# Kernel optimization log

Measured on AMD Instinct MI355X. Metric: run time of the kernel, lower is better.

Reference implementation:

```python
import jax, jax.numpy as jnp
import numpy as np

N = 50000
ALPHA = 0.1
LAMDA = 0.5


def setup_inputs() -> dict:
    key = jax.random.key(0)
    ks = jax.random.split(key, 8)
    E, IN, H, C, L = 800000, 512, 128, 40, 8
    features = jax.random.normal(ks[0], (N, IN), dtype=jnp.float32)
    edge_index = jax.random.randint(ks[1], (2, E), 0, N, dtype=jnp.int32)
    norm_A = jax.random.uniform(ks[2], (E,), dtype=jnp.float32) * 0.1
    w_fc0 = jax.random.normal(ks[3], (IN, H), dtype=jnp.float32) / np.sqrt(IN)
    b_fc0 = jnp.zeros((H,), dtype=jnp.float32)
    conv_w = jax.random.normal(ks[4], (L, H, H), dtype=jnp.float32) / np.sqrt(H)
    w_fc1 = jax.random.normal(ks[5], (H, C), dtype=jnp.float32) / np.sqrt(H)
    b_fc1 = jnp.zeros((C,), dtype=jnp.float32)
    return {"features": features, "edge_index": edge_index, "norm_A": norm_A,
            "w_fc0": w_fc0, "b_fc0": b_fc0, "conv_w": conv_w,
            "w_fc1": w_fc1, "b_fc1": b_fc1}


def _spmm(edge_index, w, x):
    # y[dst] += w_e * x[src]  over all edges; x: [N, H]
    src, dst = edge_index[0], edge_index[1]
    msgs = x[src] * w[:, None]                      # [E, H]
    return jax.ops.segment_sum(msgs, dst, num_segments=N)


def reference(features, edge_index, norm_A, w_fc0, b_fc0, conv_w, w_fc1, b_fc1):
    # dropout p=0.0 -> identity
    x = jax.nn.relu(features @ w_fc0 + b_fc0)       # [N, H]
    h0 = x
    L = conv_w.shape[0]
    for i in range(L):
        l = i + 1
        beta = jnp.log(LAMDA / l + 1.0).astype(x.dtype)
        hi = _spmm(edge_index, norm_A, x)           # Â x
        support = (1.0 - ALPHA) * hi + ALPHA * h0   # initial residual
        # identity mapping: beta * (support W) + (1-beta) * support
        x = jax.nn.relu(beta * (support @ conv_w[i]) + (1.0 - beta) * support)
    return x @ w_fc1 + b_fc1                        # [N, C]
```

## Files before the change

### kernel.cpp

```cpp
#include <hip/hip_runtime.h>
#include <hip/hip_bf16.h>
#include <math.h>

#define N_NODES 50000
#define M_PAD   50048
#define E_EDGES 800000
#define IN_DIM  512
#define HDIM    128
#define CDIM    40
#define LAYERS  8
#define NB      196

typedef __attribute__((ext_vector_type(8))) short short8;
typedef __attribute__((ext_vector_type(4))) short short4v;
typedef __attribute__((ext_vector_type(4))) float floatx4;
typedef unsigned short ushort_t;

__device__ inline float bf2f(unsigned short u) {
    return __uint_as_float(((unsigned)u) << 16);
}
__device__ inline unsigned short f2bf(float v) {
    __hip_bfloat16 b = __float2bfloat16(v);
    return *reinterpret_cast<unsigned short*>(&b);
}


__global__ void hist_kernel(const int* __restrict__ dst, int* __restrict__ cnt) {
    int i = blockIdx.x * blockDim.x + threadIdx.x;
    if (i < E_EDGES) atomicAdd(&cnt[dst[i]], 1);
}

__global__ void scanA(const int* __restrict__ cnt, int* __restrict__ bsum) {
    __shared__ int sm[256];
    int t = threadIdx.x, i = blockIdx.x * 256 + t;
    sm[t] = (i < N_NODES) ? cnt[i] : 0;
    __syncthreads();
    for (int d = 128; d > 0; d >>= 1) {
        if (t < d) sm[t] += sm[t + d];
        __syncthreads();
    }
    if (t == 0) bsum[blockIdx.x] = sm[0];
}

__global__ void scanB(const int* __restrict__ bsum, int* __restrict__ boff) {
    __shared__ int sm[256];
    int t = threadIdx.x;
    sm[t] = (t < NB) ? bsum[t] : 0;
    __syncthreads();
    for (int d = 1; d < 256; d <<= 1) {
        int v = (t >= d) ? sm[t - d] : 0;
        __syncthreads();
        sm[t] += v;
        __syncthreads();
    }
    if (t < NB) boff[t] = (t > 0) ? sm[t - 1] : 0;
}

__global__ void scanC(const int* __restrict__ cnt, const int* __restrict__ boff,
                      int* __restrict__ row_start, int* __restrict__ cursor) {
    __shared__ int sm[256];
    int t = threadIdx.x, i = blockIdx.x * 256 + t;
    int v = (i < N_NODES) ? cnt[i] : 0;
    sm[t] = v;
    __syncthreads();
    for (int d = 1; d < 256; d <<= 1) {
        int x = (t >= d) ? sm[t - d] : 0;
        __syncthreads();
        sm[t] += x;
        __syncthreads();
    }
    if (i < N_NODES) {
        int incl = boff[blockIdx.x] + sm[t];
        int excl = incl - v;
        row_start[i] = excl;
        cursor[i]    = excl;
        if (i == N_NODES - 1) row_start[N_NODES] = incl;
    }
}

__global__ void scatter_kernel(const int* __restrict__ ei, const float* __restrict__ normA,
                               int* __restrict__ cursor, int2* __restrict__ perm) {
    int i = blockIdx.x * blockDim.x + threadIdx.x;
    if (i >= E_EDGES) return;
    int d = ei[E_EDGES + i];
    int idx = atomicAdd(&cursor[d], 1);
    perm[idx] = make_int2(ei[i], __float_as_int(normA[i]));
}


__global__ void prep_weights(const float* __restrict__ W0, const float* __restrict__ convW,
                             const float* __restrict__ W1,
                             ushort_t* __restrict__ Wt0, ushort_t* __restrict__ WtL,
                             ushort_t* __restrict__ Wt1) {
    int i = blockIdx.x * blockDim.x + threadIdx.x;
    if (i < 128 * 512) {
        int n = i >> 9, k = i & 511;
        Wt0[i] = f2bf(W0[k * HDIM + n]);
        return;
    }
    int j = i - 128 * 512;
    if (j < 8 * 128 * 128) {
        int l = j >> 14, rem = j & 16383, n = rem >> 7, k = rem & 127;
        WtL[j] = f2bf(convW[l * 16384 + k * HDIM + n]);
        return;
    }
    int m = j - 8 * 128 * 128;
    if (m < 48 * 128) {
        int n = m >> 7, k = m & 127;
        Wt1[m] = (n < CDIM) ? f2bf(W1[k * CDIM + n]) : (ushort_t)0;
    }
}


__global__ __launch_bounds__(256)
void fc0_mfma(const float* __restrict__ F, const ushort_t* __restrict__ Wt0,
              const float* __restrict__ b0,
              ushort_t* __restrict__ h0b, ushort_t* __restrict__ xab) {
    int t = threadIdx.x;
    int wave = t >> 6, lane = t & 63;
    int quad = lane >> 4, l16 = lane & 15;
    int R0 = blockIdx.x * 128 + wave * 32;

    int r0 = R0 + l16;      if (r0 > N_NODES - 1) r0 = N_NODES - 1;
    int r1 = R0 + 16 + l16; if (r1 > N_NODES - 1) r1 = N_NODES - 1;
    const float* ap0 = F + (size_t)r0 * IN_DIM + quad * 8;
    const float* ap1 = F + (size_t)r1 * IN_DIM + quad * 8;
    const ushort_t* bbase = Wt0 + (size_t)l16 * IN_DIM + quad * 8;

    floatx4 acc0[8], acc1[8];
#pragma unroll
    for (int nt = 0; nt < 8; nt++) {
        acc0[nt] = (floatx4){0.f, 0.f, 0.f, 0.f};
        acc1[nt] = (floatx4){0.f, 0.f, 0.f, 0.f};
    }

    float4 pa00 = *(const float4*)(ap0);
    float4 pa01 = *(const float4*)(ap0 + 4);
    float4 pa10 = *(const float4*)(ap1);
    float4 pa11 = *(const float4*)(ap1 + 4);
    float4 pb00 = *(const float4*)(ap0 + 32);
    float4 pb01 = *(const float4*)(ap0 + 36);
    float4 pb10 = *(const float4*)(ap1 + 32);
    float4 pb11 = *(const float4*)(ap1 + 36);

#pragma unroll
    for (int kk = 0; kk < 16; kk += 2) {
        short8 a0, a1;
        a0[0] = (short)f2bf(pa00.x); a0[1] = (short)f2bf(pa00.y);
        a0[2] = (short)f2bf(pa00.z); a0[3] = (short)f2bf(pa00.w);
        a0[4] = (short)f2bf(pa01.x); a0[5] = (short)f2bf(pa01.y);
        a0[6] = (short)f2bf(pa01.z); a0[7] = (short)f2bf(pa01.w);
        a1[0] = (short)f2bf(pa10.x); a1[1] = (short)f2bf(pa10.y);
        a1[2] = (short)f2bf(pa10.z); a1[3] = (short)f2bf(pa10.w);
        a1[4] = (short)f2bf(pa11.x); a1[5] = (short)f2bf(pa11.y);
        a1[6] = (short)f2bf(pa11.z); a1[7] = (short)f2bf(pa11.w);
        if (kk + 2 < 16) {
            pa00 = *(const float4*)(ap0 + (kk + 2) * 32);
            pa01 = *(const float4*)(ap0 + (kk + 2) * 32 + 4);
            pa10 = *(const float4*)(ap1 + (kk + 2) * 32);
            pa11 = *(const float4*)(ap1 + (kk + 2) * 32 + 4);
        }
#pragma unroll
        for (int nt = 0; nt < 8; nt++) {
            short8 b = *(const short8*)(bbase + (size_t)nt * 16 * IN_DIM + kk * 32);
            acc0[nt] = __builtin_amdgcn_mfma_f32_16x16x32_bf16(a0, b, acc0[nt], 0, 0, 0);
            acc1[nt] = __builtin_amdgcn_mfma_f32_16x16x32_bf16(a1, b, acc1[nt], 0, 0, 0);
        }
        short8 c0, c1;
        c0[0] = (short)f2bf(pb00.x); c0[1] = (short)f2bf(pb00.y);
        c0[2] = (short)f2bf(pb00.z); c0[3] = (short)f2bf(pb00.w);
        c0[4] = (short)f2bf(pb01.x); c0[5] = (short)f2bf(pb01.y);
        c0[6] = (short)f2bf(pb01.z); c0[7] = (short)f2bf(pb01.w);
        c1[0] = (short)f2bf(pb10.x); c1[1] = (short)f2bf(pb10.y);
        c1[2] = (short)f2bf(pb10.z); c1[3] = (short)f2bf(pb10.w);
        c1[4] = (short)f2bf(pb11.x); c1[5] = (short)f2bf(pb11.y);
        c1[6] = (short)f2bf(pb11.z); c1[7] = (short)f2bf(pb11.w);
        if (kk + 3 < 16) {
            pb00 = *(const float4*)(ap0 + (kk + 3) * 32);
            pb01 = *(const float4*)(ap0 + (kk + 3) * 32 + 4);
            pb10 = *(const float4*)(ap1 + (kk + 3) * 32);
            pb11 = *(const float4*)(ap1 + (kk + 3) * 32 + 4);
        }
#pragma unroll
        for (int nt = 0; nt < 8; nt++) {
            short8 b = *(const short8*)(bbase + (size_t)nt * 16 * IN_DIM + (kk + 1) * 32);
            acc0[nt] = __builtin_amdgcn_mfma_f32_16x16x32_bf16(c0, b, acc0[nt], 0, 0, 0);
            acc1[nt] = __builtin_amdgcn_mfma_f32_16x16x32_bf16(c1, b, acc1[nt], 0, 0, 0);
        }
    }

#pragma unroll
    for (int nt = 0; nt < 8; nt++) {
        int col = nt * 16 + l16;
        float bias = b0[col];
#pragma unroll
        for (int r = 0; r < 4; r++) {
            int row = R0 + quad * 4 + r;
            float v = acc0[nt][r] + bias;
            v = v > 0.f ? v : 0.f;
            ushort_t u = f2bf(v);
            h0b[(size_t)row * HDIM + col] = u;
            xab[(size_t)row * HDIM + col] = u;
        }
#pragma unroll
        for (int r = 0; r < 4; r++) {
            int row = R0 + 16 + quad * 4 + r;
            float v = acc1[nt][r] + bias;
            v = v > 0.f ? v : 0.f;
            ushort_t u = f2bf(v);
            h0b[(size_t)row * HDIM + col] = u;
            xab[(size_t)row * HDIM + col] = u;
        }
    }
}


#define SROW 136

__global__ void layer_fused(const int* __restrict__ row_start, const int2* __restrict__ perm,
                            const ushort_t* __restrict__ xb, const ushort_t* __restrict__ h0b,
                            const ushort_t* __restrict__ Wt, ushort_t* __restrict__ X,
                            float beta) {
    __shared__ short sS[64][SROW];
    int t = threadIdx.x;
    int wave = t >> 6, lane = t & 63;
    int slot = lane >> 4, sl = lane & 15;
    int quad = slot, l16 = sl;
    int row0 = blockIdx.x * 64;
    int R0 = row0 + wave * 16;

    int rb = 0;
    if (lane <= 16) {
        int idx = R0 + lane;
        if (idx > N_NODES) idx = N_NODES;
        rb = row_start[idx];
    }

    for (int r = 0; r < 16; r++) {
        int e0 = __shfl(rb, r), e1 = __shfl(rb, r + 1);
        int grow = R0 + r;
        float acc[8];
#pragma unroll
        for (int c = 0; c < 8; c++) acc[c] = 0.f;

        int ebase = e0 + slot;
        int2 m[4];
        short8 v[4];
#pragma unroll
        for (int d = 0; d < 4; d++) {
            int e = ebase + 4 * d;
            m[d] = (e < e1) ? perm[e] : make_int2(0, 0);
        }
#pragma unroll
        for (int d = 0; d < 4; d++) {
            int e = ebase + 4 * d;
            if (e < e1) v[d] = *(const short8*)(xb + (size_t)m[d].x * HDIM + sl * 8);
        }
        for (int e = ebase; e < e1; e += 16) {
            int2 mn[4];
#pragma unroll
            for (int d = 0; d < 4; d++) {
                int en = e + 16 + 4 * d;
                mn[d] = (en < e1) ? perm[en] : make_int2(0, 0);
            }
#pragma unroll
            for (int d = 0; d < 4; d++) {
                int ec = e + 4 * d;
                if (ec < e1) {
                    float w = __int_as_float(m[d].y);
#pragma unroll
                    for (int c = 0; c < 8; c++) acc[c] += w * bf2f((ushort_t)v[d][c]);
                }
            }
#pragma unroll
            for (int d = 0; d < 4; d++) {
                int en = e + 16 + 4 * d;
                if (en < e1) v[d] = *(const short8*)(xb + (size_t)mn[d].x * HDIM + sl * 8);
                m[d] = mn[d];
            }
        }
#pragma unroll
        for (int c = 0; c < 8; c++) {
            acc[c] += __shfl_xor(acc[c], 16);
            acc[c] += __shfl_xor(acc[c], 32);
        }
        if (slot == 0) {
            short8 o;
            if (grow < N_NODES) {
                short8 h = *(const short8*)(h0b + (size_t)grow * HDIM + sl * 8);
#pragma unroll
                for (int c = 0; c < 8; c++)
                    o[c] = (short)f2bf(0.9f * acc[c] + 0.1f * bf2f((ushort_t)h[c]));
            } else {
#pragma unroll
                for (int c = 0; c < 8; c++) o[c] = 0;
            }
            *(short8*)&sS[wave * 16 + r][sl * 8] = o;
        }
    }
    __syncthreads();

    short8 afrag[4];
#pragma unroll
    for (int ks = 0; ks < 4; ks++)
        afrag[ks] = *(const short8*)&sS[wave * 16 + l16][ks * 32 + quad * 8];

    floatx4 gacc[8];
#pragma unroll
    for (int nt = 0; nt < 8; nt++) {
        const ushort_t* bp = Wt + (size_t)(nt * 16 + l16) * HDIM + quad * 8;
        floatx4 c = (floatx4){0.f, 0.f, 0.f, 0.f};
#pragma unroll
        for (int ks = 0; ks < 4; ks++) {
            short8 b = *(const short8*)(bp + ks * 32);
            c = __builtin_amdgcn_mfma_f32_16x16x32_bf16(afrag[ks], b, c, 0, 0, 0);
        }
        gacc[nt] = c;
    }
    float g = 1.f - beta;
#pragma unroll
    for (int nt = 0; nt < 8; nt++) {
        int col = nt * 16 + l16;
#pragma unroll
        for (int r = 0; r < 4; r++) {
            int lrow = wave * 16 + quad * 4 + r;
            float s = bf2f((ushort_t)sS[lrow][col]);
            float v = beta * gacc[nt][r] + g * s;
            v = v > 0.f ? v : 0.f;
            X[(size_t)(row0 + lrow) * HDIM + col] = f2bf(v);
        }
    }
}


__global__ void fc1_mfma(const ushort_t* __restrict__ X, const ushort_t* __restrict__ Wt1,
                         const float* __restrict__ b1, float* __restrict__ out) {
    int wave = threadIdx.x >> 6;
    int lane = threadIdx.x & 63;
    int quad = lane >> 4, l16 = lane & 15;
    int row0 = blockIdx.x * 64 + wave * 16;

    int arow = row0 + l16; if (arow > N_NODES - 1) arow = N_NODES - 1;
    const ushort_t* ap = X + (size_t)arow * HDIM + quad * 8;
    short8 afrag[4];
#pragma unroll
    for (int ks = 0; ks < 4; ks++) afrag[ks] = *(const short8*)(ap + ks * 32);

    floatx4 acc[3];
#pragma unroll
    for (int nt = 0; nt < 3; nt++) {
        const ushort_t* bp = Wt1 + (size_t)(nt * 16 + l16) * HDIM + quad * 8;
        floatx4 c = (floatx4){0.f, 0.f, 0.f, 0.f};
#pragma unroll
        for (int ks = 0; ks < 4; ks++) {
            short8 b = *(const short8*)(bp + ks * 32);
            c = __builtin_amdgcn_mfma_f32_16x16x32_bf16(afrag[ks], b, c, 0, 0, 0);
        }
        acc[nt] = c;
    }
#pragma unroll
    for (int nt = 0; nt < 3; nt++) {
        int col = nt * 16 + l16;
        if (col < CDIM) {
            float bias = b1[col];
#pragma unroll
            for (int r = 0; r < 4; r++) {
                int row = row0 + quad * 4 + r;
                if (row < N_NODES)
                    out[(size_t)row * CDIM + col] = acc[nt][r] + bias;
            }
        }
    }
}


extern "C" void kernel_launch(void* const* d_in, const int* in_sizes, int n_in,
                              void* d_out, int out_size, void* d_ws, size_t ws_size,
                              hipStream_t stream) {
    const float* F     = (const float*)d_in[0];
    const int*   ei    = (const int*)d_in[1];
    const float* normA = (const float*)d_in[2];
    const float* W0    = (const float*)d_in[3];
    const float* b0    = (const float*)d_in[4];
    const float* convW = (const float*)d_in[5];
    const float* W1    = (const float*)d_in[6];
    const float* b1    = (const float*)d_in[7];
    float*       out   = (float*)d_out;

    ushort_t* h0b  = (ushort_t*)d_ws;
    ushort_t* xab  = h0b + (size_t)M_PAD * HDIM;
    ushort_t* xbb  = xab + (size_t)M_PAD * HDIM;
    ushort_t* Wt0  = xbb + (size_t)M_PAD * HDIM;
    ushort_t* WtL  = Wt0 + 128 * 512;
    ushort_t* Wt1  = WtL + 8 * 128 * 128;
    int*   row_start = (int*)(Wt1 + 48 * 128);
    int*   cursor    = row_start + (N_NODES + 8);
    int*   cnt       = cursor + (N_NODES + 8);
    int*   bsum      = cnt + (N_NODES + 8);
    int*   boff      = bsum + 256;
    int2*  perm      = (int2*)(boff + 256);

    hipMemsetAsync(cnt, 0, N_NODES * sizeof(int), stream);
    hist_kernel<<<(E_EDGES + 255) / 256, 256, 0, stream>>>(ei + E_EDGES, cnt);
    scanA<<<NB, 256, 0, stream>>>(cnt, bsum);
    scanB<<<1, 256, 0, stream>>>(bsum, boff);
    scanC<<<NB, 256, 0, stream>>>(cnt, boff, row_start, cursor);
    scatter_kernel<<<(E_EDGES + 255) / 256, 256, 0, stream>>>(ei, normA, cursor, perm);
    prep_weights<<<(128 * 512 + 8 * 128 * 128 + 48 * 128 + 255) / 256, 256, 0, stream>>>(
        W0, convW, W1, Wt0, WtL, Wt1);

    fc0_mfma<<<M_PAD / 128, 256, 0, stream>>>(F, Wt0, b0, h0b, xab);

    ushort_t* ping = xab;
    ushort_t* pong = xbb;
    for (int i = 0; i < LAYERS; i++) {
        float beta = logf(0.5f / (float)(i + 1) + 1.0f);
        layer_fused<<<M_PAD / 64, 256, 0, stream>>>(
            row_start, perm, ping, h0b, WtL + (size_t)i * HDIM * HDIM, pong, beta);
        ushort_t* tmp = ping; ping = pong; pong = tmp;
    }
    fc1_mfma<<<M_PAD / 64, 256, 0, stream>>>(xab, Wt1, b1, out);
}
```

Measured before the change: 786.2 us.

## Assign rows to 16-lane groups in SpMM gather and drop duplicate fc0 store

The sparse aggregation now gives each 16-lane group four rows instead of one wave per row split across four slots. Edge indices are loaded cooperatively and broadcast with width-16 shuffles. This removes the cross-slot shuffle reduction and the idle lanes on low-degree rows, but drops the explicit software prefetch pipeline. fc0 also no longer writes a duplicate copy of h0, and the first layer reads h0b directly.

```diff
diff --git a/kernel.cpp b/kernel.cpp
--- a/kernel.cpp
+++ b/kernel.cpp
@@ -12,7 +12,6 @@
 #define NB      196
 
 typedef __attribute__((ext_vector_type(8))) short short8;
-typedef __attribute__((ext_vector_type(4))) short short4v;
 typedef __attribute__((ext_vector_type(4))) float floatx4;
 typedef unsigned short ushort_t;
 
@@ -114,8 +113,7 @@
 
 __global__ __launch_bounds__(256)
 void fc0_mfma(const float* __restrict__ F, const ushort_t* __restrict__ Wt0,
-              const float* __restrict__ b0,
-              ushort_t* __restrict__ h0b, ushort_t* __restrict__ xab) {
+              const float* __restrict__ b0, ushort_t* __restrict__ h0b) {
     int t = threadIdx.x;
     int wave = t >> 6, lane = t & 63;
     int quad = lane >> 4, l16 = lane & 15;
@@ -198,18 +196,14 @@
             int row = R0 + quad * 4 + r;
             float v = acc0[nt][r] + bias;
             v = v > 0.f ? v : 0.f;
-            ushort_t u = f2bf(v);
-            h0b[(size_t)row * HDIM + col] = u;
-            xab[(size_t)row * HDIM + col] = u;
+            h0b[(size_t)row * HDIM + col] = f2bf(v);
         }
 #pragma unroll
         for (int r = 0; r < 4; r++) {
             int row = R0 + 16 + quad * 4 + r;
             float v = acc1[nt][r] + bias;
             v = v > 0.f ? v : 0.f;
-            ushort_t u = f2bf(v);
-            h0b[(size_t)row * HDIM + col] = u;
-            xab[(size_t)row * HDIM + col] = u;
+            h0b[(size_t)row * HDIM + col] = f2bf(v);
         }
     }
 }
@@ -217,86 +211,69 @@
 
 #define SROW 136
 
-__global__ void layer_fused(const int* __restrict__ row_start, const int2* __restrict__ perm,
-                            const ushort_t* __restrict__ xb, const ushort_t* __restrict__ h0b,
-                            const ushort_t* __restrict__ Wt, ushort_t* __restrict__ X,
-                            float beta) {
+__global__ __launch_bounds__(256)
+void layer_fused(const int* __restrict__ row_start, const int2* __restrict__ perm,
+                 const ushort_t* __restrict__ xb, const ushort_t* __restrict__ h0b,
+                 const ushort_t* __restrict__ Wt, ushort_t* __restrict__ X,
+                 float beta) {
     __shared__ short sS[64][SROW];
     int t = threadIdx.x;
     int wave = t >> 6, lane = t & 63;
-    int slot = lane >> 4, sl = lane & 15;
-    int quad = slot, l16 = sl;
+    int grp = lane >> 4, sl = lane & 15;
+    int quad = lane >> 4, l16 = lane & 15;
     int row0 = blockIdx.x * 64;
-    int R0 = row0 + wave * 16;
-
-    int rb = 0;
-    if (lane <= 16) {
-        int idx = R0 + lane;
-        if (idx > N_NODES) idx = N_NODES;
-        rb = row_start[idx];
-    }
-
-    for (int r = 0; r < 16; r++) {
-        int e0 = __shfl(rb, r), e1 = __shfl(rb, r + 1);
-        int grow = R0 + r;
+    int G = wave * 4 + grp;
+    int Rg = row0 + G * 4;
+
+    for (int r = 0; r < 4; r++) {
+        int row = Rg + r;
+        int i0 = row < N_NODES ? row : N_NODES;
+        int i1 = row + 1 < N_NODES ? row + 1 : N_NODES;
+        int e0 = row_start[i0];
+        int e1 = row_start[i1];
+
         float acc[8];
 #pragma unroll
         for (int c = 0; c < 8; c++) acc[c] = 0.f;
 
-        int ebase = e0 + slot;
-        int2 m[4];
-        short8 v[4];
-#pragma unroll
-        for (int d = 0; d < 4; d++) {
-            int e = ebase + 4 * d;
-            m[d] = (e < e1) ? perm[e] : make_int2(0, 0);
-        }
-#pragma unroll
-        for (int d = 0; d < 4; d++) {
-            int e = ebase + 4 * d;
-            if (e < e1) v[d] = *(const short8*)(xb + (size_t)m[d].x * HDIM + sl * 8);
-        }
-        for (int e = ebase; e < e1; e += 16) {
-            int2 mn[4];
-#pragma unroll
-            for (int d = 0; d < 4; d++) {
-                int en = e + 16 + 4 * d;
-                mn[d] = (en < e1) ? perm[en] : make_int2(0, 0);
-            }
-#pragma unroll
-            for (int d = 0; d < 4; d++) {
-                int ec = e + 4 * d;
-                if (ec < e1) {
-                    float w = __int_as_float(m[d].y);
-#pragma unroll
-                    for (int c = 0; c < 8; c++) acc[c] += w * bf2f((ushort_t)v[d][c]);
+        for (int chunk = e0; chunk < e1; chunk += 16) {
+            int2 pm = make_int2(0, 0);
+            if (chunk + sl < e1) pm = perm[chunk + sl];
+#pragma unroll
+            for (int d = 0; d < 16; d += 4) {
+                int   s0 = __shfl(pm.x, d + 0, 16);
+                int   s1 = __shfl(pm.x, d + 1, 16);
+                int   s2 = __shfl(pm.x, d + 2, 16);
+                int   s3 = __shfl(pm.x, d + 3, 16);
+                float w0 = __int_as_float(__shfl(pm.y, d + 0, 16));
+                float w1 = __int_as_float(__shfl(pm.y, d + 1, 16));
+                float w2 = __int_as_float(__shfl(pm.y, d + 2, 16));
+                float w3 = __int_as_float(__shfl(pm.y, d + 3, 16));
+                short8 v0 = *(const short8*)(xb + (size_t)s0 * HDIM + sl * 8);
+                short8 v1 = *(const short8*)(xb + (size_t)s1 * HDIM + sl * 8);
+                short8 v2 = *(const short8*)(xb + (size_t)s2 * HDIM + sl * 8);
+                short8 v3 = *(const short8*)(xb + (size_t)s3 * HDIM + sl * 8);
+#pragma unroll
+                for (int c = 0; c < 8; c++) {
+                    acc[c] += w0 * bf2f((ushort_t)v0[c]);
+                    acc[c] += w1 * bf2f((ushort_t)v1[c]);
+                    acc[c] += w2 * bf2f((ushort_t)v2[c]);
+                    acc[c] += w3 * bf2f((ushort_t)v3[c]);
                 }
             }
-#pragma unroll
-            for (int d = 0; d < 4; d++) {
-                int en = e + 16 + 4 * d;
-                if (en < e1) v[d] = *(const short8*)(xb + (size_t)mn[d].x * HDIM + sl * 8);
-                m[d] = mn[d];
-            }
-        }
-#pragma unroll
-        for (int c = 0; c < 8; c++) {
-            acc[c] += __shfl_xor(acc[c], 16);
-            acc[c] += __shfl_xor(acc[c], 32);
-        }
-        if (slot == 0) {
-            short8 o;
-            if (grow < N_NODES) {
-                short8 h = *(const short8*)(h0b + (size_t)grow * HDIM + sl * 8);
-#pragma unroll
-                for (int c = 0; c < 8; c++)
-                    o[c] = (short)f2bf(0.9f * acc[c] + 0.1f * bf2f((ushort_t)h[c]));
-            } else {
-#pragma unroll
-                for (int c = 0; c < 8; c++) o[c] = 0;
-            }
-            *(short8*)&sS[wave * 16 + r][sl * 8] = o;
-        }
+        }
+
+        short8 o;
+        if (row < N_NODES) {
+            short8 h = *(const short8*)(h0b + (size_t)row * HDIM + sl * 8);
+#pragma unroll
+            for (int c = 0; c < 8; c++)
+                o[c] = (short)f2bf(0.9f * acc[c] + 0.1f * bf2f((ushort_t)h[c]));
+        } else {
+#pragma unroll
+            for (int c = 0; c < 8; c++) o[c] = 0;
+        }
+        *(short8*)&sS[G * 4 + r][sl * 8] = o;
     }
     __syncthreads();
 
@@ -409,15 +386,16 @@
     prep_weights<<<(128 * 512 + 8 * 128 * 128 + 48 * 128 + 255) / 256, 256, 0, stream>>>(
         W0, convW, W1, Wt0, WtL, Wt1);
 
-    fc0_mfma<<<M_PAD / 128, 256, 0, stream>>>(F, Wt0, b0, h0b, xab);
-
-    ushort_t* ping = xab;
-    ushort_t* pong = xbb;
+    fc0_mfma<<<M_PAD / 128, 256, 0, stream>>>(F, Wt0, b0, h0b);
+
+    ushort_t* ping = h0b;
+    ushort_t* pong = xab;
     for (int i = 0; i < LAYERS; i++) {
         float beta = logf(0.5f / (float)(i + 1) + 1.0f);
         layer_fused<<<M_PAD / 64, 256, 0, stream>>>(
             row_start, perm, ping, h0b, WtL + (size_t)i * HDIM * HDIM, pong, beta);
-        ushort_t* tmp = ping; ping = pong; pong = tmp;
-    }
-    fc1_mfma<<<M_PAD / 64, 256, 0, stream>>>(xab, Wt1, b1, out);
-}
+        if (i == 0) { ping = xab; pong = xbb; }
+        else { ushort_t* tmp = ping; ping = pong; pong = tmp; }
+    }
+    fc1_mfma<<<M_PAD / 64, 256, 0, stream>>>(ping, Wt1, b1, out);
+}
```

New measurement: 732.1 us. 1.07x faster.
